# Optimization experiments

Measured on AMD Instinct MI355X. Metric: run time of the kernel, lower is better.

## Reference

```python
import jax, jax.numpy as jnp
import numpy as np

IN_F = 128
OUT_F = 128
HEADS = 2
N_NODES = 50000
N_EDGES = 400000


def setup_inputs() -> dict:
    key = jax.random.key(0)
    ks = jax.random.split(key, 5)
    x = jax.random.normal(ks[0], (N_NODES, IN_F), dtype=jnp.float32)
    edge_index = jax.random.randint(ks[1], (2, N_EDGES), 0, N_NODES, dtype=jnp.int64)
    # Per-head linear weights (Kaiming-uniform-ish) and xavier bilinear weights
    lim = 1.0 / np.sqrt(IN_F)
    W_lin = jax.random.uniform(ks[2], (HEADS, OUT_F, IN_F), minval=-lim, maxval=lim, dtype=jnp.float32)
    b_lin = jax.random.uniform(ks[3], (HEADS, OUT_F), minval=-lim, maxval=lim, dtype=jnp.float32)
    xav = 1.414 * np.sqrt(6.0 / (OUT_F + OUT_F))
    W_att = jax.random.uniform(ks[4], (HEADS, OUT_F, OUT_F), minval=-xav, maxval=xav, dtype=jnp.float32)
    return {"x": x, "edge_index": edge_index, "W_lin": W_lin, "b_lin": b_lin, "W_att": W_att}


def reference(x, edge_index, W_lin, b_lin, W_att):
    row, col = edge_index[0], edge_index[1]
    # head_x: [H, N, O] -- per-head linear projection
    head_x = jnp.einsum('nd,hod->hno', x, W_lin) + b_lin[:, None, :]
    hr = head_x[:, row]  # [H, E, O] source-node features per edge
    hc = head_x[:, col]  # [H, E, O] target-node features per edge
    # per-edge bilinear form: diag(hr @ W @ hc.T) == sum((hr @ W) * hc, -1)
    scores = jnp.einsum('heo,hop,hep->he', hr, W_att, hc)  # [H, E]
    return jax.nn.sigmoid(scores.mean(axis=0))  # [E]
```

## Files before the change

kernel.cpp:

```cpp
#include <hip/hip_runtime.h>
#include <hip/hip_fp16.h>

constexpr int N_NODES = 50000;
constexpr int N_EDGES = 400000;
constexpr int F = 128;

constexpr int NBUK  = 512;
constexpr int EPB   = 1024;
constexpr int NBLK  = (N_EDGES + EPB - 1) / EPB;
constexpr int NBLKP = 392;

typedef _Float16 f16x8 __attribute__((ext_vector_type(8)));
typedef _Float16 f16x4 __attribute__((ext_vector_type(4)));
typedef _Float16 f16x2 __attribute__((ext_vector_type(2)));
typedef float    f32x4 __attribute__((ext_vector_type(4)));

union v8v2 { f16x8 v8; f16x2 v2[4]; };

__device__ __forceinline__ int swz(int row, int colh) {
    return (row * F + colh) ^ ((row & 7) << 3);
}


__global__ __launch_bounds__(256) void gat_fuse1(
    const float* __restrict__ W_lin, const float* __restrict__ b_lin,
    const float* __restrict__ W_att,
    float* __restrict__ Wfws, float* __restrict__ w1ws, float* __restrict__ w2ws)
{
    __shared__ float wl[128][8];
    __shared__ float bl[128];
    const int h  = blockIdx.x >> 4;
    const int cb = blockIdx.x & 15;
    const int t  = threadIdx.x;
    const float* WL = W_lin + h * F * F;
    const float* WA = W_att + h * F * F;

    {   int p = t >> 1, d0 = (t & 1) * 4;
        float4 v = *(const float4*)(WL + p * F + cb * 8 + d0);
        wl[p][d0+0]=v.x; wl[p][d0+1]=v.y; wl[p][d0+2]=v.z; wl[p][d0+3]=v.w;
    }
    if (t < 128) bl[t] = b_lin[h * F + t];
    __syncthreads();

    {
        int o = t >> 1, j2 = (t & 1) * 4;
        float a0=0, a1=0, a2=0, a3=0;
        const float* war = WA + o * F;
        #pragma unroll 4
        for (int p = 0; p < F; ++p) {
            float wa = war[p];
            a0 += wa * wl[p][j2+0]; a1 += wa * wl[p][j2+1];
            a2 += wa * wl[p][j2+2]; a3 += wa * wl[p][j2+3];
        }
        float4 fv = {a0, a1, a2, a3};
        *(float4*)(Wfws + h * F * F + o * F + cb * 8 + j2) = fv;
    }

    if (cb == 0) {
        if (t < 128) {
            float s = 0;
            #pragma unroll 4
            for (int o = 0; o < F; ++o) s += WA[o * F + t] * bl[o];
            w1ws[h * F + t] = s;
        } else {
            int o = t - 128;
            float s = 0;
            const float* war = WA + o * F;
            #pragma unroll 4
            for (int p = 0; p < F; ++p) s += war[p] * bl[p];
            w2ws[h * F + o] = s;
        }
    }
}

__global__ __launch_bounds__(256) void gat_fuse2(
    const float* __restrict__ W_lin, const float* __restrict__ b_lin,
    const float* __restrict__ Wfws,
    const float* __restrict__ w1ws, const float* __restrict__ w2ws,
    _Float16* __restrict__ Mall, float* __restrict__ uvws)
{
    __shared__ float wlh[128 * 128];
    __shared__ float wfs[128][8];
    __shared__ float red[256];
    const int cb = blockIdx.x;
    const int t  = threadIdx.x;
    const int i  = t >> 1, j2 = (t & 1) * 4;

    float acc0=0, acc1=0, acc2=0, acc3=0;
    float puv = 0;
    const int ii = t & 127;

    for (int h = 0; h < 2; ++h) {
        __syncthreads();
        const float* WL = W_lin + h * F * F;
        #pragma unroll
        for (int q = 0; q < 16; ++q) {
            int idx = (q * 256 + t) * 4;
            *(float4*)(wlh + idx) = *(const float4*)(WL + idx);
        }
        {   int o = t >> 1, jb = (t & 1) * 4;
            float4 v = *(const float4*)(Wfws + h * F * F + o * F + cb * 8 + jb);
            wfs[o][jb+0]=v.x; wfs[o][jb+1]=v.y; wfs[o][jb+2]=v.z; wfs[o][jb+3]=v.w;
        }
        __syncthreads();
        #pragma unroll 4
        for (int o = 0; o < F; ++o) {
            float wv = wlh[o * F + i];
            acc0 += wv * wfs[o][j2+0];
            acc1 += wv * wfs[o][j2+1];
            acc2 += wv * wfs[o][j2+2];
            acc3 += wv * wfs[o][j2+3];
        }
        if (cb == 0) {
            const float* wsrc = (t < 128) ? (w1ws + h * F) : (w2ws + h * F);
            #pragma unroll 4
            for (int o = 0; o < F; ++o) puv += wlh[o * F + ii] * wsrc[o];
        }
    }

    f16x4 hv;
    hv[0]=(_Float16)acc0; hv[1]=(_Float16)acc1;
    hv[2]=(_Float16)acc2; hv[3]=(_Float16)acc3;
    *(f16x4*)(Mall + i * F + cb * 8 + j2) = hv;

    if (cb == 0) {
        uvws[(t < 128 ? 0 : 128) + ii] = puv;
        int hh = t >> 7, oo = t & 127;
        red[t] = b_lin[hh * F + oo] * w2ws[hh * F + oo];
        __syncthreads();
        #pragma unroll
        for (int d = 128; d > 0; d >>= 1) {
            if (t < d) red[t] += red[t + d];
            __syncthreads();
        }
        if (t == 0) uvws[256] = red[0];
    }
}

__global__ __launch_bounds__(256) void gat_hist(
    const int* __restrict__ ei, unsigned* __restrict__ bcnt)
{
    __shared__ unsigned h[NBUK];
    const int t = threadIdx.x, b = blockIdx.x;
    h[t] = 0; h[t + 256] = 0;
    __syncthreads();
    const int base = b * EPB;
    #pragma unroll
    for (int i = 0; i < EPB / 256; ++i) {
        int e = base + i * 256 + t;
        if (e < N_EDGES) atomicAdd(&h[(unsigned)ei[e] >> 7], 1u);
    }
    __syncthreads();
    bcnt[t * NBLKP + b]         = h[t];
    bcnt[(t + 256) * NBLKP + b] = h[t + 256];
}

__global__ __launch_bounds__(512) void gat_scan_row(
    const unsigned* __restrict__ bcnt, unsigned* __restrict__ bof,
    unsigned* __restrict__ btot)
{
    __shared__ unsigned s[512];
    const int B = blockIdx.x, t = threadIdx.x;
    unsigned v = (t < NBLK) ? bcnt[B * NBLKP + t] : 0u;
    s[t] = v;
    __syncthreads();
    #pragma unroll
    for (int d = 1; d < 512; d <<= 1) {
        unsigned u = (t >= d) ? s[t - d] : 0u;
        __syncthreads();
        s[t] += u;
        __syncthreads();
    }
    if (t < NBLK) bof[B * NBLKP + t] = s[t] - v;
    if (t == 511) btot[B] = s[511];
}

__global__ __launch_bounds__(512) void gat_scan_bkt(
    const unsigned* __restrict__ btot, unsigned* __restrict__ bbase)
{
    __shared__ unsigned s[NBUK];
    const int t = threadIdx.x;
    unsigned v = btot[t];
    s[t] = v;
    __syncthreads();
    #pragma unroll
    for (int d = 1; d < NBUK; d <<= 1) {
        unsigned u = (t >= d) ? s[t - d] : 0u;
        __syncthreads();
        s[t] += u;
        __syncthreads();
    }
    bbase[t] = s[t] - v;
}

__global__ __launch_bounds__(256) void gat_scatter(
    const int* __restrict__ ei, const unsigned* __restrict__ bof,
    const unsigned* __restrict__ bbase, uint2* __restrict__ sorted)
{
    __shared__ unsigned base[NBUK];
    const int t = threadIdx.x, b = blockIdx.x;
    base[t]       = bof[t * NBLKP + b] + bbase[t];
    base[t + 256] = bof[(t + 256) * NBLKP + b] + bbase[t + 256];
    __syncthreads();
    const int bs = b * EPB;
    #pragma unroll
    for (int i = 0; i < EPB / 256; ++i) {
        int e = bs + i * 256 + t;
        if (e < N_EDGES) {
            unsigned r = (unsigned)ei[e], c = (unsigned)ei[N_EDGES + e];
            unsigned pos = atomicAdd(&base[r >> 7], 1u);
            sorted[pos] = make_uint2(r | (c << 16), (unsigned)e);
        }
    }
}

__global__ __launch_bounds__(256) void gat_gemm(
    const float* __restrict__ x,
    const _Float16* __restrict__ Mall,
    const float* __restrict__ uvws,
    _Float16* __restrict__ XH, _Float16* __restrict__ Z,
    float* __restrict__ su, float* __restrict__ sv)
{
    __shared__ _Float16 wbuf[F * F];
    __shared__ _Float16 stag[4][16 * F];

    const int t    = threadIdx.x;
    const int wave = t >> 6;
    const int lane = t & 63;
    const int r16  = lane & 15;
    const int kgrp = lane >> 4;
    const int node_base = blockIdx.x * 64 + wave * 16;

    #pragma unroll
    for (int i = 0; i < 8; ++i) {
        int idx8 = i * 256 + t;
        *(f16x8*)(wbuf + swz(idx8 >> 4, (idx8 & 15) * 8)) =
            *(const f16x8*)(Mall + (size_t)idx8 * 8);
    }

    f16x8 xf[4];
    {
        int xrow = node_base + r16;
        if (xrow >= N_NODES) xrow = N_NODES - 1;
        const float* xp = x + (size_t)xrow * F + kgrp * 8;
        #pragma unroll
        for (int kk = 0; kk < 4; ++kk) {
            float4 v0 = *(const float4*)(xp + kk * 32);
            float4 v1 = *(const float4*)(xp + kk * 32 + 4);
            f16x8 hv;
            hv[0]=(_Float16)v0.x; hv[1]=(_Float16)v0.y;
            hv[2]=(_Float16)v0.z; hv[3]=(_Float16)v0.w;
            hv[4]=(_Float16)v1.x; hv[5]=(_Float16)v1.y;
            hv[6]=(_Float16)v1.z; hv[7]=(_Float16)v1.w;
            xf[kk] = hv;
        }
    }
    __syncthreads();

    const int node = node_base + r16;

    #pragma unroll
    for (int c = 0; c < 8; ++c) {
        f16x8 aw[4];
        #pragma unroll
        for (int kk = 0; kk < 4; ++kk)
            aw[kk] = *(const f16x8*)(wbuf + swz(c * 16 + r16, kk * 32 + kgrp * 8));
        f32x4 acc = {0.f, 0.f, 0.f, 0.f};
        #pragma unroll
        for (int kk = 0; kk < 4; ++kk)
            acc = __builtin_amdgcn_mfma_f32_16x16x32_f16(aw[kk], xf[kk], acc, 0, 0, 0);
        f16x4 hv;
        hv[0]=(_Float16)acc[0]; hv[1]=(_Float16)acc[1];
        hv[2]=(_Float16)acc[2]; hv[3]=(_Float16)acc[3];
        *(f16x4*)(&stag[wave][swz(r16, c * 16 + kgrp * 4)]) = hv;
    }
    {
        int nd = lane >> 2;
        int node2 = node_base + nd;
        #pragma unroll
        for (int i = 0; i < 4; ++i) {
            int f0 = (lane & 3) * 8 + i * 32;
            f16x8 v = *(const f16x8*)(&stag[wave][swz(nd, f0)]);
            if (node2 < N_NODES)
                *(f16x8*)(Z + (size_t)node2 * F + f0) = v;
        }
    }
    {
        #pragma unroll
        for (int kk = 0; kk < 4; ++kk)
            *(f16x8*)(&stag[wave][swz(r16, kk * 32 + kgrp * 8)]) = xf[kk];
        int nd = lane >> 2;
        int node2 = node_base + nd;
        #pragma unroll
        for (int i = 0; i < 4; ++i) {
            int f0 = (lane & 3) * 8 + i * 32;
            f16x8 v = *(const f16x8*)(&stag[wave][swz(nd, f0)]);
            if (node2 < N_NODES)
                *(f16x8*)(XH + (size_t)node2 * F + f0) = v;
        }
    }
    {
        float pu = 0.f, pv = 0.f;
        #pragma unroll
        for (int kk = 0; kk < 4; ++kk) {
            int kb = kgrp * 8 + kk * 32;
            float4 u0 = *(const float4*)(uvws + kb);
            float4 u1 = *(const float4*)(uvws + kb + 4);
            float4 v0 = *(const float4*)(uvws + 128 + kb);
            float4 v1 = *(const float4*)(uvws + 128 + kb + 4);
            pu += u0.x*(float)xf[kk][0] + u0.y*(float)xf[kk][1]
                + u0.z*(float)xf[kk][2] + u0.w*(float)xf[kk][3]
                + u1.x*(float)xf[kk][4] + u1.y*(float)xf[kk][5]
                + u1.z*(float)xf[kk][6] + u1.w*(float)xf[kk][7];
            pv += v0.x*(float)xf[kk][0] + v0.y*(float)xf[kk][1]
                + v0.z*(float)xf[kk][2] + v0.w*(float)xf[kk][3]
                + v1.x*(float)xf[kk][4] + v1.y*(float)xf[kk][5]
                + v1.z*(float)xf[kk][6] + v1.w*(float)xf[kk][7];
        }
        pu += __shfl_xor(pu, 16); pu += __shfl_xor(pu, 32);
        pv += __shfl_xor(pv, 16); pv += __shfl_xor(pv, 32);
        if (kgrp == 0 && node < N_NODES) {
            su[node] = pu + uvws[256];
            sv[node] = pv;
        }
    }
}

__global__ __launch_bounds__(256) void gat_edge(
    const uint2* __restrict__ sorted,
    const _Float16* __restrict__ XH, const _Float16* __restrict__ Z,
    const float* __restrict__ su, const float* __restrict__ sv,
    float* __restrict__ out)
{
    const int nwg = gridDim.x;
    int bid = blockIdx.x;
    int xcd = bid & 7, loc = bid >> 3;
    int q = nwg >> 3, rr = nwg & 7;
    int wg = (xcd < rr ? xcd * (q + 1) : rr * (q + 1) + (xcd - rr) * q) + loc;

    int lane = threadIdx.x & 63;
    int idx  = wg * 64 + (threadIdx.x >> 6) * 16 + (lane >> 2);
    int hl   = lane & 3;
    if (idx >= N_EDGES) return;

    uint2 rc = sorted[idx];
    int r = rc.x & 0xFFFF;
    int c = rc.x >> 16;

    const _Float16* hp = XH + (size_t)r * F + hl * 32;
    const _Float16* ap = Z  + (size_t)c * F + hl * 32;
    v8v2 a[4], b[4];
    #pragma unroll
    for (int i = 0; i < 4; ++i) a[i].v8 = *(const f16x8*)(hp + i * 8);
    #pragma unroll
    for (int i = 0; i < 4; ++i) b[i].v8 = *(const f16x8*)(ap + i * 8);

    float p = 0.f;
    #pragma unroll
    for (int i = 0; i < 4; ++i)
        #pragma unroll
        for (int j = 0; j < 4; ++j)
            p = __builtin_amdgcn_fdot2(a[i].v2[j], b[i].v2[j], p, false);

    p += __shfl_xor(p, 1);
    p += __shfl_xor(p, 2);

    if (hl == 0) {
        float s = p + su[c] + sv[r];
        out[rc.y] = 1.f / (1.f + __expf(-0.5f * s));
    }
}

extern "C" void kernel_launch(void* const* d_in, const int* in_sizes, int n_in,
                              void* d_out, int out_size, void* d_ws, size_t ws_size,
                              hipStream_t stream) {
    const float* x     = (const float*)d_in[0];
    const int*   ei    = (const int*)d_in[1];
    const float* W_lin = (const float*)d_in[2];
    const float* b_lin = (const float*)d_in[3];
    const float* W_att = (const float*)d_in[4];
    float* out = (float*)d_out;

    float*    Wfws  = (float*)d_ws;
    float*    w1ws  = Wfws + 2 * F * F;
    float*    w2ws  = w1ws + 2 * F;
    float*    uvws  = w2ws + 2 * F;
    _Float16* Mall  = (_Float16*)(uvws + 512);
    _Float16* XH    = Mall + F * F;
    _Float16* Z     = XH + (size_t)N_NODES * F;
    float*    su    = (float*)(Z + (size_t)N_NODES * F);
    float*    sv    = su + N_NODES;
    unsigned* bcnt  = (unsigned*)(sv + N_NODES);
    unsigned* bof   = bcnt + NBUK * NBLKP;
    unsigned* btot  = bof + NBUK * NBLKP;
    unsigned* bbase = btot + NBUK;
    uint2*    sorted= (uint2*)(bbase + NBUK);

    gat_hist<<<NBLK, 256, 0, stream>>>(ei, bcnt);
    gat_scan_row<<<NBUK, 512, 0, stream>>>(bcnt, bof, btot);
    gat_scan_bkt<<<1, NBUK, 0, stream>>>(btot, bbase);
    gat_scatter<<<NBLK, 256, 0, stream>>>(ei, bof, bbase, sorted);

    gat_fuse1<<<32, 256, 0, stream>>>(W_lin, b_lin, W_att, Wfws, w1ws, w2ws);
    gat_fuse2<<<16, 256, 0, stream>>>(W_lin, b_lin, Wfws, w1ws, w2ws, Mall, uvws);
    gat_gemm<<<(N_NODES + 63) / 64, 256, 0, stream>>>(x, Mall, uvws, XH, Z, su, sv);

    gat_edge<<<N_EDGES / 64, 256, 0, stream>>>(sorted, XH, Z, su, sv, out);
}
```

Before: 81.36 us.

## Drop edge bucket sort and merge weight-fusion kernels into one

Removes the histogram/scan/scatter pipeline that sorted edges by source-node bucket, so the edge kernel now reads edge indices directly and writes outputs in natural order. The two precompute kernels that fold W_att into W_lin are merged into one kernel that recomputes the fused slice per block. This cuts several kernel launches and the sort's memory traffic, at the cost of less locality in the random row gathers of XH during the edge pass.

```diff
diff --git a/kernel.cpp b/kernel.cpp
--- a/kernel.cpp
+++ b/kernel.cpp
@@ -4,11 +4,6 @@
 constexpr int N_NODES = 50000;
 constexpr int N_EDGES = 400000;
 constexpr int F = 128;
-
-constexpr int NBUK  = 512;
-constexpr int EPB   = 1024;
-constexpr int NBLK  = (N_EDGES + EPB - 1) / EPB;
-constexpr int NBLKP = 392;
 
 typedef _Float16 f16x8 __attribute__((ext_vector_type(8)));
 typedef _Float16 f16x4 __attribute__((ext_vector_type(4)));
@@ -21,88 +16,68 @@
     return (row * F + colh) ^ ((row & 7) << 3);
 }
 
-
-__global__ __launch_bounds__(256) void gat_fuse1(
+__global__ __launch_bounds__(256) void gat_fuse(
     const float* __restrict__ W_lin, const float* __restrict__ b_lin,
     const float* __restrict__ W_att,
-    float* __restrict__ Wfws, float* __restrict__ w1ws, float* __restrict__ w2ws)
-{
-    __shared__ float wl[128][8];
-    __shared__ float bl[128];
-    const int h  = blockIdx.x >> 4;
-    const int cb = blockIdx.x & 15;
-    const int t  = threadIdx.x;
-    const float* WL = W_lin + h * F * F;
-    const float* WA = W_att + h * F * F;
-
-    {   int p = t >> 1, d0 = (t & 1) * 4;
-        float4 v = *(const float4*)(WL + p * F + cb * 8 + d0);
-        wl[p][d0+0]=v.x; wl[p][d0+1]=v.y; wl[p][d0+2]=v.z; wl[p][d0+3]=v.w;
-    }
-    if (t < 128) bl[t] = b_lin[h * F + t];
-    __syncthreads();
-
-    {
-        int o = t >> 1, j2 = (t & 1) * 4;
-        float a0=0, a1=0, a2=0, a3=0;
-        const float* war = WA + o * F;
-        #pragma unroll 4
-        for (int p = 0; p < F; ++p) {
-            float wa = war[p];
-            a0 += wa * wl[p][j2+0]; a1 += wa * wl[p][j2+1];
-            a2 += wa * wl[p][j2+2]; a3 += wa * wl[p][j2+3];
-        }
-        float4 fv = {a0, a1, a2, a3};
-        *(float4*)(Wfws + h * F * F + o * F + cb * 8 + j2) = fv;
-    }
-
-    if (cb == 0) {
-        if (t < 128) {
-            float s = 0;
-            #pragma unroll 4
-            for (int o = 0; o < F; ++o) s += WA[o * F + t] * bl[o];
-            w1ws[h * F + t] = s;
-        } else {
-            int o = t - 128;
-            float s = 0;
-            const float* war = WA + o * F;
-            #pragma unroll 4
-            for (int p = 0; p < F; ++p) s += war[p] * bl[p];
-            w2ws[h * F + o] = s;
-        }
-    }
-}
-
-__global__ __launch_bounds__(256) void gat_fuse2(
-    const float* __restrict__ W_lin, const float* __restrict__ b_lin,
-    const float* __restrict__ Wfws,
-    const float* __restrict__ w1ws, const float* __restrict__ w2ws,
     _Float16* __restrict__ Mall, float* __restrict__ uvws)
 {
-    __shared__ float wlh[128 * 128];
-    __shared__ float wfs[128][8];
+    __shared__ float wlh[F * F];
+    __shared__ float wfs[F][8];
+    __shared__ float bl[F];
+    __shared__ float w12[2 * F];
     __shared__ float red[256];
+
     const int cb = blockIdx.x;
     const int t  = threadIdx.x;
     const int i  = t >> 1, j2 = (t & 1) * 4;
-
-    float acc0=0, acc1=0, acc2=0, acc3=0;
+    const int ii = t & 127;
+
+    float acc0 = 0, acc1 = 0, acc2 = 0, acc3 = 0;
     float puv = 0;
-    const int ii = t & 127;
+    float c0s = 0;
 
     for (int h = 0; h < 2; ++h) {
         __syncthreads();
         const float* WL = W_lin + h * F * F;
+        const float* WA = W_att + h * F * F;
         #pragma unroll
         for (int q = 0; q < 16; ++q) {
             int idx = (q * 256 + t) * 4;
             *(float4*)(wlh + idx) = *(const float4*)(WL + idx);
         }
-        {   int o = t >> 1, jb = (t & 1) * 4;
-            float4 v = *(const float4*)(Wfws + h * F * F + o * F + cb * 8 + jb);
-            wfs[o][jb+0]=v.x; wfs[o][jb+1]=v.y; wfs[o][jb+2]=v.z; wfs[o][jb+3]=v.w;
-        }
+        if (t < F) bl[t] = b_lin[h * F + t];
         __syncthreads();
+
+        {
+            int o = t >> 1, jb = (t & 1) * 4;
+            float a0=0, a1=0, a2=0, a3=0;
+            const float* war = WA + o * F;
+            #pragma unroll 4
+            for (int p = 0; p < F; ++p) {
+                float wa = war[p];
+                const float* wr = wlh + p * F + cb * 8 + jb;
+                a0 += wa * wr[0]; a1 += wa * wr[1];
+                a2 += wa * wr[2]; a3 += wa * wr[3];
+            }
+            wfs[o][jb+0]=a0; wfs[o][jb+1]=a1; wfs[o][jb+2]=a2; wfs[o][jb+3]=a3;
+        }
+        if (cb == 0) {
+            if (t < F) {
+                float s = 0;
+                #pragma unroll 4
+                for (int o = 0; o < F; ++o) s += WA[o * F + t] * bl[o];
+                w12[t] = s;
+            } else {
+                int o = t - F;
+                float s = 0;
+                const float* war = WA + o * F;
+                #pragma unroll 4
+                for (int p = 0; p < F; ++p) s += war[p] * bl[p];
+                w12[F + o] = s;
+            }
+        }
+        __syncthreads();
+
         #pragma unroll 4
         for (int o = 0; o < F; ++o) {
             float wv = wlh[o * F + i];
@@ -112,9 +87,17 @@
             acc3 += wv * wfs[o][j2+3];
         }
         if (cb == 0) {
-            const float* wsrc = (t < 128) ? (w1ws + h * F) : (w2ws + h * F);
+            const float* wsrc = (t < F) ? w12 : (w12 + F);
             #pragma unroll 4
             for (int o = 0; o < F; ++o) puv += wlh[o * F + ii] * wsrc[o];
+            red[t] = (t < F) ? bl[t] * w12[F + t] : 0.f;
+            __syncthreads();
+            #pragma unroll
+            for (int d = 128; d > 0; d >>= 1) {
+                if (t < d) red[t] += red[t + d];
+                __syncthreads();
+            }
+            if (t == 0) c0s += red[0];
         }
     }
 
@@ -124,93 +107,8 @@
     *(f16x4*)(Mall + i * F + cb * 8 + j2) = hv;
 
     if (cb == 0) {
-        uvws[(t < 128 ? 0 : 128) + ii] = puv;
-        int hh = t >> 7, oo = t & 127;
-        red[t] = b_lin[hh * F + oo] * w2ws[hh * F + oo];
-        __syncthreads();
-        #pragma unroll
-        for (int d = 128; d > 0; d >>= 1) {
-            if (t < d) red[t] += red[t + d];
-            __syncthreads();
-        }
-        if (t == 0) uvws[256] = red[0];
-    }
-}
-
-__global__ __launch_bounds__(256) void gat_hist(
-    const int* __restrict__ ei, unsigned* __restrict__ bcnt)
-{
-    __shared__ unsigned h[NBUK];
-    const int t = threadIdx.x, b = blockIdx.x;
-    h[t] = 0; h[t + 256] = 0;
-    __syncthreads();
-    const int base = b * EPB;
-    #pragma unroll
-    for (int i = 0; i < EPB / 256; ++i) {
-        int e = base + i * 256 + t;
-        if (e < N_EDGES) atomicAdd(&h[(unsigned)ei[e] >> 7], 1u);
-    }
-    __syncthreads();
-    bcnt[t * NBLKP + b]         = h[t];
-    bcnt[(t + 256) * NBLKP + b] = h[t + 256];
-}
-
-__global__ __launch_bounds__(512) void gat_scan_row(
-    const unsigned* __restrict__ bcnt, unsigned* __restrict__ bof,
-    unsigned* __restrict__ btot)
-{
-    __shared__ unsigned s[512];
-    const int B = blockIdx.x, t = threadIdx.x;
-    unsigned v = (t < NBLK) ? bcnt[B * NBLKP + t] : 0u;
-    s[t] = v;
-    __syncthreads();
-    #pragma unroll
-    for (int d = 1; d < 512; d <<= 1) {
-        unsigned u = (t >= d) ? s[t - d] : 0u;
-        __syncthreads();
-        s[t] += u;
-        __syncthreads();
-    }
-    if (t < NBLK) bof[B * NBLKP + t] = s[t] - v;
-    if (t == 511) btot[B] = s[511];
-}
-
-__global__ __launch_bounds__(512) void gat_scan_bkt(
-    const unsigned* __restrict__ btot, unsigned* __restrict__ bbase)
-{
-    __shared__ unsigned s[NBUK];
-    const int t = threadIdx.x;
-    unsigned v = btot[t];
-    s[t] = v;
-    __syncthreads();
-    #pragma unroll
-    for (int d = 1; d < NBUK; d <<= 1) {
-        unsigned u = (t >= d) ? s[t - d] : 0u;
-        __syncthreads();
-        s[t] += u;
-        __syncthreads();
-    }
-    bbase[t] = s[t] - v;
-}
-
-__global__ __launch_bounds__(256) void gat_scatter(
-    const int* __restrict__ ei, const unsigned* __restrict__ bof,
-    const unsigned* __restrict__ bbase, uint2* __restrict__ sorted)
-{
-    __shared__ unsigned base[NBUK];
-    const int t = threadIdx.x, b = blockIdx.x;
-    base[t]       = bof[t * NBLKP + b] + bbase[t];
-    base[t + 256] = bof[(t + 256) * NBLKP + b] + bbase[t + 256];
-    __syncthreads();
-    const int bs = b * EPB;
-    #pragma unroll
-    for (int i = 0; i < EPB / 256; ++i) {
-        int e = bs + i * 256 + t;
-        if (e < N_EDGES) {
-            unsigned r = (unsigned)ei[e], c = (unsigned)ei[N_EDGES + e];
-            unsigned pos = atomicAdd(&base[r >> 7], 1u);
-            sorted[pos] = make_uint2(r | (c << 16), (unsigned)e);
-        }
+        uvws[(t < F ? 0 : F) + ii] = puv;
+        if (t == 0) uvws[256] = c0s;
     }
 }
 
@@ -327,25 +225,18 @@
 }
 
 __global__ __launch_bounds__(256) void gat_edge(
-    const uint2* __restrict__ sorted,
+    const int* __restrict__ ei,
     const _Float16* __restrict__ XH, const _Float16* __restrict__ Z,
     const float* __restrict__ su, const float* __restrict__ sv,
     float* __restrict__ out)
 {
-    const int nwg = gridDim.x;
-    int bid = blockIdx.x;
-    int xcd = bid & 7, loc = bid >> 3;
-    int q = nwg >> 3, rr = nwg & 7;
-    int wg = (xcd < rr ? xcd * (q + 1) : rr * (q + 1) + (xcd - rr) * q) + loc;
-
-    int lane = threadIdx.x & 63;
-    int idx  = wg * 64 + (threadIdx.x >> 6) * 16 + (lane >> 2);
-    int hl   = lane & 3;
-    if (idx >= N_EDGES) return;
-
-    uint2 rc = sorted[idx];
-    int r = rc.x & 0xFFFF;
-    int c = rc.x >> 16;
+    int gid = blockIdx.x * 256 + threadIdx.x;
+    int e   = gid >> 2;
+    int hl  = threadIdx.x & 3;
+    if (e >= N_EDGES) return;
+
+    int r = ei[e];
+    int c = ei[N_EDGES + e];
 
     const _Float16* hp = XH + (size_t)r * F + hl * 32;
     const _Float16* ap = Z  + (size_t)c * F + hl * 32;
@@ -367,7 +258,7 @@
 
     if (hl == 0) {
         float s = p + su[c] + sv[r];
-        out[rc.y] = 1.f / (1.f + __expf(-0.5f * s));
+        out[e] = 1.f / (1.f + __expf(-0.5f * s));
     }
 }
 
@@ -381,29 +272,14 @@
     const float* W_att = (const float*)d_in[4];
     float* out = (float*)d_out;
 
-    float*    Wfws  = (float*)d_ws;
-    float*    w1ws  = Wfws + 2 * F * F;
-    float*    w2ws  = w1ws + 2 * F;
-    float*    uvws  = w2ws + 2 * F;
-    _Float16* Mall  = (_Float16*)(uvws + 512);
-    _Float16* XH    = Mall + F * F;
-    _Float16* Z     = XH + (size_t)N_NODES * F;
-    float*    su    = (float*)(Z + (size_t)N_NODES * F);
-    float*    sv    = su + N_NODES;
-    unsigned* bcnt  = (unsigned*)(sv + N_NODES);
-    unsigned* bof   = bcnt + NBUK * NBLKP;
-    unsigned* btot  = bof + NBUK * NBLKP;
-    unsigned* bbase = btot + NBUK;
-    uint2*    sorted= (uint2*)(bbase + NBUK);
-
-    gat_hist<<<NBLK, 256, 0, stream>>>(ei, bcnt);
-    gat_scan_row<<<NBUK, 512, 0, stream>>>(bcnt, bof, btot);
-    gat_scan_bkt<<<1, NBUK, 0, stream>>>(btot, bbase);
-    gat_scatter<<<NBLK, 256, 0, stream>>>(ei, bof, bbase, sorted);
-
-    gat_fuse1<<<32, 256, 0, stream>>>(W_lin, b_lin, W_att, Wfws, w1ws, w2ws);
-    gat_fuse2<<<16, 256, 0, stream>>>(W_lin, b_lin, Wfws, w1ws, w2ws, Mall, uvws);
+    _Float16* Mall = (_Float16*)d_ws;
+    float*    uvws = (float*)(Mall + F * F);
+    _Float16* XH   = (_Float16*)(uvws + 512);
+    _Float16* Z    = XH + (size_t)N_NODES * F;
+    float*    su   = (float*)(Z + (size_t)N_NODES * F);
+    float*    sv   = su + N_NODES;
+
+    gat_fuse<<<16, 256, 0, stream>>>(W_lin, b_lin, W_att, Mall, uvws);
     gat_gemm<<<(N_NODES + 63) / 64, 256, 0, stream>>>(x, Mall, uvws, XH, Z, su, sv);
-
-    gat_edge<<<N_EDGES / 64, 256, 0, stream>>>(sorted, XH, Z, su, sv, out);
-}
+    gat_edge<<<(N_EDGES * 4 + 255) / 256, 256, 0, stream>>>(ei, XH, Z, su, sv, out);
+}
```

Result: faster. 72.04 us (-11.5%).

## Sort edges by 2D (row, col) tile key and fuse weight-folding kernels

Applied to the files above, without the earlier changes.

Edges are now bucketed by a 2D key built from the high bits of both source and target node (4096 buckets instead of 512 row-only buckets). This aims to improve cache locality for both the XH and Z gathers in the edge kernel. The two weight-folding kernels are merged into one, so the intermediate workspace round-trip and one launch go away, at the cost of each block recomputing its slice. The bigger histogram raises scan work (4096 row scans) and the shared memory used by hist and scatter.

```diff
diff --git a/kernel.cpp b/kernel.cpp
--- a/kernel.cpp
+++ b/kernel.cpp
@@ -5,7 +5,7 @@
 constexpr int N_EDGES = 400000;
 constexpr int F = 128;
 
-constexpr int NBUK  = 512;
+constexpr int NBUK2 = 4096;
 constexpr int EPB   = 1024;
 constexpr int NBLK  = (N_EDGES + EPB - 1) / EPB;
 constexpr int NBLKP = 392;
@@ -21,88 +21,71 @@
     return (row * F + colh) ^ ((row & 7) << 3);
 }
 
-
-__global__ __launch_bounds__(256) void gat_fuse1(
+__device__ __forceinline__ unsigned ekey(unsigned r, unsigned c) {
+    return ((r >> 13) << 9) | (c >> 7);
+}
+
+__global__ __launch_bounds__(256) void gat_fuse(
     const float* __restrict__ W_lin, const float* __restrict__ b_lin,
     const float* __restrict__ W_att,
-    float* __restrict__ Wfws, float* __restrict__ w1ws, float* __restrict__ w2ws)
-{
-    __shared__ float wl[128][8];
-    __shared__ float bl[128];
-    const int h  = blockIdx.x >> 4;
-    const int cb = blockIdx.x & 15;
-    const int t  = threadIdx.x;
-    const float* WL = W_lin + h * F * F;
-    const float* WA = W_att + h * F * F;
-
-    {   int p = t >> 1, d0 = (t & 1) * 4;
-        float4 v = *(const float4*)(WL + p * F + cb * 8 + d0);
-        wl[p][d0+0]=v.x; wl[p][d0+1]=v.y; wl[p][d0+2]=v.z; wl[p][d0+3]=v.w;
-    }
-    if (t < 128) bl[t] = b_lin[h * F + t];
-    __syncthreads();
-
-    {
-        int o = t >> 1, j2 = (t & 1) * 4;
-        float a0=0, a1=0, a2=0, a3=0;
-        const float* war = WA + o * F;
-        #pragma unroll 4
-        for (int p = 0; p < F; ++p) {
-            float wa = war[p];
-            a0 += wa * wl[p][j2+0]; a1 += wa * wl[p][j2+1];
-            a2 += wa * wl[p][j2+2]; a3 += wa * wl[p][j2+3];
-        }
-        float4 fv = {a0, a1, a2, a3};
-        *(float4*)(Wfws + h * F * F + o * F + cb * 8 + j2) = fv;
-    }
-
-    if (cb == 0) {
-        if (t < 128) {
-            float s = 0;
-            #pragma unroll 4
-            for (int o = 0; o < F; ++o) s += WA[o * F + t] * bl[o];
-            w1ws[h * F + t] = s;
-        } else {
-            int o = t - 128;
-            float s = 0;
-            const float* war = WA + o * F;
-            #pragma unroll 4
-            for (int p = 0; p < F; ++p) s += war[p] * bl[p];
-            w2ws[h * F + o] = s;
-        }
-    }
-}
-
-__global__ __launch_bounds__(256) void gat_fuse2(
-    const float* __restrict__ W_lin, const float* __restrict__ b_lin,
-    const float* __restrict__ Wfws,
-    const float* __restrict__ w1ws, const float* __restrict__ w2ws,
     _Float16* __restrict__ Mall, float* __restrict__ uvws)
 {
-    __shared__ float wlh[128 * 128];
-    __shared__ float wfs[128][8];
+    __shared__ float wlh[F * F];
+    __shared__ float wfs[F][8];
+    __shared__ float bl[F];
+    __shared__ float w12[2 * F];
     __shared__ float red[256];
+
     const int cb = blockIdx.x;
     const int t  = threadIdx.x;
     const int i  = t >> 1, j2 = (t & 1) * 4;
-
-    float acc0=0, acc1=0, acc2=0, acc3=0;
+    const int ii = t & 127;
+
+    float acc0 = 0, acc1 = 0, acc2 = 0, acc3 = 0;
     float puv = 0;
-    const int ii = t & 127;
+    float c0s = 0;
 
     for (int h = 0; h < 2; ++h) {
         __syncthreads();
         const float* WL = W_lin + h * F * F;
+        const float* WA = W_att + h * F * F;
         #pragma unroll
         for (int q = 0; q < 16; ++q) {
             int idx = (q * 256 + t) * 4;
             *(float4*)(wlh + idx) = *(const float4*)(WL + idx);
         }
+        if (t < F) bl[t] = b_lin[h * F + t];
+        __syncthreads();
+
         {   int o = t >> 1, jb = (t & 1) * 4;
-            float4 v = *(const float4*)(Wfws + h * F * F + o * F + cb * 8 + jb);
-            wfs[o][jb+0]=v.x; wfs[o][jb+1]=v.y; wfs[o][jb+2]=v.z; wfs[o][jb+3]=v.w;
-        }
-        __syncthreads();
+            float a0=0, a1=0, a2=0, a3=0;
+            const float* war = WA + o * F;
+            #pragma unroll 4
+            for (int p = 0; p < F; ++p) {
+                float wa = war[p];
+                const float* wr = wlh + p * F + cb * 8 + jb;
+                a0 += wa * wr[0]; a1 += wa * wr[1];
+                a2 += wa * wr[2]; a3 += wa * wr[3];
+            }
+            wfs[o][jb+0]=a0; wfs[o][jb+1]=a1; wfs[o][jb+2]=a2; wfs[o][jb+3]=a3;
+        }
+        if (cb == 0) {
+            if (t < F) {
+                float s = 0;
+                #pragma unroll 4
+                for (int o = 0; o < F; ++o) s += WA[o * F + t] * bl[o];
+                w12[t] = s;
+            } else {
+                int o = t - F;
+                float s = 0;
+                const float* war = WA + o * F;
+                #pragma unroll 4
+                for (int p = 0; p < F; ++p) s += war[p] * bl[p];
+                w12[F + o] = s;
+            }
+        }
+        __syncthreads();
+
         #pragma unroll 4
         for (int o = 0; o < F; ++o) {
             float wv = wlh[o * F + i];
@@ -112,9 +95,17 @@
             acc3 += wv * wfs[o][j2+3];
         }
         if (cb == 0) {
-            const float* wsrc = (t < 128) ? (w1ws + h * F) : (w2ws + h * F);
+            const float* wsrc = (t < F) ? w12 : (w12 + F);
             #pragma unroll 4
             for (int o = 0; o < F; ++o) puv += wlh[o * F + ii] * wsrc[o];
+            red[t] = (t < F) ? bl[t] * w12[F + t] : 0.f;
+            __syncthreads();
+            #pragma unroll
+            for (int d = 128; d > 0; d >>= 1) {
+                if (t < d) red[t] += red[t + d];
+                __syncthreads();
+            }
+            if (t == 0) c0s += red[0];
         }
     }
 
@@ -124,35 +115,30 @@
     *(f16x4*)(Mall + i * F + cb * 8 + j2) = hv;
 
     if (cb == 0) {
-        uvws[(t < 128 ? 0 : 128) + ii] = puv;
-        int hh = t >> 7, oo = t & 127;
-        red[t] = b_lin[hh * F + oo] * w2ws[hh * F + oo];
-        __syncthreads();
-        #pragma unroll
-        for (int d = 128; d > 0; d >>= 1) {
-            if (t < d) red[t] += red[t + d];
-            __syncthreads();
-        }
-        if (t == 0) uvws[256] = red[0];
+        uvws[(t < F ? 0 : F) + ii] = puv;
+        if (t == 0) uvws[256] = c0s;
     }
 }
 
 __global__ __launch_bounds__(256) void gat_hist(
     const int* __restrict__ ei, unsigned* __restrict__ bcnt)
 {
-    __shared__ unsigned h[NBUK];
+    __shared__ unsigned h[NBUK2];
     const int t = threadIdx.x, b = blockIdx.x;
-    h[t] = 0; h[t + 256] = 0;
+    #pragma unroll
+    for (int i = 0; i < NBUK2 / 256; ++i) h[t + i * 256] = 0;
     __syncthreads();
     const int base = b * EPB;
     #pragma unroll
     for (int i = 0; i < EPB / 256; ++i) {
         int e = base + i * 256 + t;
-        if (e < N_EDGES) atomicAdd(&h[(unsigned)ei[e] >> 7], 1u);
-    }
-    __syncthreads();
-    bcnt[t * NBLKP + b]         = h[t];
-    bcnt[(t + 256) * NBLKP + b] = h[t + 256];
+        if (e < N_EDGES)
+            atomicAdd(&h[ekey((unsigned)ei[e], (unsigned)ei[N_EDGES + e])], 1u);
+    }
+    __syncthreads();
+    #pragma unroll
+    for (int i = 0; i < NBUK2 / 256; ++i)
+        bcnt[(t + i * 256) * NBLKP + b] = h[t + i * 256];
 }
 
 __global__ __launch_bounds__(512) void gat_scan_row(
@@ -178,29 +164,37 @@
 __global__ __launch_bounds__(512) void gat_scan_bkt(
     const unsigned* __restrict__ btot, unsigned* __restrict__ bbase)
 {
-    __shared__ unsigned s[NBUK];
+    __shared__ unsigned s[512];
     const int t = threadIdx.x;
-    unsigned v = btot[t];
-    s[t] = v;
-    __syncthreads();
-    #pragma unroll
-    for (int d = 1; d < NBUK; d <<= 1) {
+    unsigned loc[8];
+    unsigned sum = 0;
+    #pragma unroll
+    for (int j = 0; j < 8; ++j) { loc[j] = btot[t * 8 + j]; sum += loc[j]; }
+    s[t] = sum;
+    __syncthreads();
+    #pragma unroll
+    for (int d = 1; d < 512; d <<= 1) {
         unsigned u = (t >= d) ? s[t - d] : 0u;
         __syncthreads();
         s[t] += u;
         __syncthreads();
     }
-    bbase[t] = s[t] - v;
+    unsigned run = s[t] - sum;
+    #pragma unroll
+    for (int j = 0; j < 8; ++j) { bbase[t * 8 + j] = run; run += loc[j]; }
 }
 
 __global__ __launch_bounds__(256) void gat_scatter(
     const int* __restrict__ ei, const unsigned* __restrict__ bof,
     const unsigned* __restrict__ bbase, uint2* __restrict__ sorted)
 {
-    __shared__ unsigned base[NBUK];
+    __shared__ unsigned base[NBUK2];
     const int t = threadIdx.x, b = blockIdx.x;
-    base[t]       = bof[t * NBLKP + b] + bbase[t];
-    base[t + 256] = bof[(t + 256) * NBLKP + b] + bbase[t + 256];
+    #pragma unroll
+    for (int i = 0; i < NBUK2 / 256; ++i) {
+        int B = t + i * 256;
+        base[B] = bof[B * NBLKP + b] + bbase[B];
+    }
     __syncthreads();
     const int bs = b * EPB;
     #pragma unroll
@@ -208,7 +202,7 @@
         int e = bs + i * 256 + t;
         if (e < N_EDGES) {
             unsigned r = (unsigned)ei[e], c = (unsigned)ei[N_EDGES + e];
-            unsigned pos = atomicAdd(&base[r >> 7], 1u);
+            unsigned pos = atomicAdd(&base[ekey(r, c)], 1u);
             sorted[pos] = make_uint2(r | (c << 16), (unsigned)e);
         }
     }
@@ -338,9 +332,8 @@
     int q = nwg >> 3, rr = nwg & 7;
     int wg = (xcd < rr ? xcd * (q + 1) : rr * (q + 1) + (xcd - rr) * q) + loc;
 
-    int lane = threadIdx.x & 63;
-    int idx  = wg * 64 + (threadIdx.x >> 6) * 16 + (lane >> 2);
-    int hl   = lane & 3;
+    int idx = wg * 64 + (threadIdx.x >> 2);
+    int hl  = threadIdx.x & 3;
     if (idx >= N_EDGES) return;
 
     uint2 rc = sorted[idx];
@@ -381,29 +374,24 @@
     const float* W_att = (const float*)d_in[4];
     float* out = (float*)d_out;
 
-    float*    Wfws  = (float*)d_ws;
-    float*    w1ws  = Wfws + 2 * F * F;
-    float*    w2ws  = w1ws + 2 * F;
-    float*    uvws  = w2ws + 2 * F;
-    _Float16* Mall  = (_Float16*)(uvws + 512);
-    _Float16* XH    = Mall + F * F;
+    _Float16* Mall  = (_Float16*)d_ws;
+    float*    uvws  = (float*)(Mall + F * F);
+    _Float16* XH    = (_Float16*)(uvws + 512);
     _Float16* Z     = XH + (size_t)N_NODES * F;
     float*    su    = (float*)(Z + (size_t)N_NODES * F);
     float*    sv    = su + N_NODES;
     unsigned* bcnt  = (unsigned*)(sv + N_NODES);
-    unsigned* bof   = bcnt + NBUK * NBLKP;
-    unsigned* btot  = bof + NBUK * NBLKP;
-    unsigned* bbase = btot + NBUK;
-    uint2*    sorted= (uint2*)(bbase + NBUK);
-
+    unsigned* bof   = bcnt + (size_t)NBUK2 * NBLKP;
+    unsigned* btot  = bof + (size_t)NBUK2 * NBLKP;
+    unsigned* bbase = btot + NBUK2;
+    uint2*    sorted= (uint2*)(bbase + NBUK2);
+
+    gat_fuse<<<16, 256, 0, stream>>>(W_lin, b_lin, W_att, Mall, uvws);
     gat_hist<<<NBLK, 256, 0, stream>>>(ei, bcnt);
-    gat_scan_row<<<NBUK, 512, 0, stream>>>(bcnt, bof, btot);
-    gat_scan_bkt<<<1, NBUK, 0, stream>>>(btot, bbase);
+    gat_scan_row<<<NBUK2, 512, 0, stream>>>(bcnt, bof, btot);
+    gat_scan_bkt<<<1, 512, 0, stream>>>(btot, bbase);
     gat_scatter<<<NBLK, 256, 0, stream>>>(ei, bof, bbase, sorted);
 
-    gat_fuse1<<<32, 256, 0, stream>>>(W_lin, b_lin, W_att, Wfws, w1ws, w2ws);
-    gat_fuse2<<<16, 256, 0, stream>>>(W_lin, b_lin, Wfws, w1ws, w2ws, Mall, uvws);
     gat_gemm<<<(N_NODES + 63) / 64, 256, 0, stream>>>(x, Mall, uvws, XH, Z, su, sv);
-
-    gat_edge<<<N_EDGES / 64, 256, 0, stream>>>(sorted, XH, Z, su, sv, out);
-}
+    gat_edge<<<(N_EDGES + 63) / 64, 256, 0, stream>>>(sorted, XH, Z, su, sv, out);
+}
```

Result: slower. 111.6 us (+37.1%).
